# Performance work log

Hardware: AMD Instinct MI355X
Metric: run time of the kernel (lower is better)

## Reference

```python
import jax, jax.numpy as jnp
import numpy as np

EMBED_DIM = 1024
NUM_HEADS = 16
HEAD_DIM = EMBED_DIM // NUM_HEADS


def setup_inputs() -> dict:
    key = jax.random.key(0)
    ks = jax.random.split(key, 11)
    B, S, D = 4, 2048, EMBED_DIM
    s = 1.0 / np.sqrt(D)
    return {
        "q": jax.random.normal(ks[0], (B, S, D), jnp.float32),
        "k": jax.random.normal(ks[1], (B, S, D), jnp.float32),
        "v": jax.random.normal(ks[2], (B, S, D), jnp.float32),
        "Wq": jax.random.normal(ks[3], (D, D), jnp.float32) * s,
        "bq": jnp.zeros((D,), jnp.float32),
        "Wk": jax.random.normal(ks[4], (D, D), jnp.float32) * s,
        "bk": jnp.zeros((D,), jnp.float32),
        "Wv": jax.random.normal(ks[5], (D, D), jnp.float32) * s,
        "bv": jnp.zeros((D,), jnp.float32),
        "Wo": jax.random.normal(ks[6], (D, D), jnp.float32) * s,
        "bo": jnp.zeros((D,), jnp.float32),
    }


def reference(q, k, v, Wq, bq, Wk, bk, Wv, bv, Wo, bo):
    B, S, D = q.shape
    H, Hd = NUM_HEADS, HEAD_DIM
    # projections, split heads -> [B, H, S, Hd]
    qh = (q @ Wq + bq).reshape(B, S, H, Hd).transpose(0, 2, 1, 3)
    kh = (k @ Wk + bk).reshape(B, S, H, Hd).transpose(0, 2, 1, 3)
    vh = (v @ Wv + bv).reshape(B, S, H, Hd).transpose(0, 2, 1, 3)
    scale = 1.0 / jnp.sqrt(jnp.asarray(Hd, qh.dtype))
    scores = jnp.einsum('bhqd,bhkd->bhqk', qh, kh) * scale  # [B,H,S,S]
    attn = jax.nn.softmax(scores, axis=-1)  # dropout = identity in eval
    out = jnp.einsum('bhqk,bhkd->bhqd', attn, vh)
    out = out.transpose(0, 2, 1, 3).reshape(B, S, D)
    return out @ Wo + bo
```

## Files before the change

kernel.cpp:

```cpp
#include <hip/hip_runtime.h>

typedef __attribute__((ext_vector_type(8))) __bf16 bf16x8;
typedef __attribute__((ext_vector_type(4))) __bf16 bf16x4;
typedef __attribute__((ext_vector_type(4))) float f32x4;
typedef __attribute__((ext_vector_type(16))) float f32x16;
typedef __attribute__((ext_vector_type(4))) unsigned int u32x4;

#define GLDS(g, l) __builtin_amdgcn_global_load_lds( \
    (const __attribute__((address_space(1))) void*)(g), \
    (__attribute__((address_space(3))) void*)(l), 16, 0, 0)

__device__ __forceinline__ unsigned cvtpk_bf16(float lo, float hi) {
    unsigned r;
    asm("v_cvt_pk_bf16_f32 %0, %1, %2" : "=v"(r) : "v"(lo), "v"(hi));
    return r;
}
__device__ __forceinline__ void pl32swap(unsigned& a, unsigned& b) {
    asm("v_permlane32_swap_b32 %0, %1" : "+v"(a), "+v"(b));
}

__global__ __launch_bounds__(256) void cvt_tile(const float* __restrict__ q,
                                                const float* __restrict__ k,
                                                const float* __restrict__ v,
                                                __bf16* __restrict__ qo,
                                                __bf16* __restrict__ ko,
                                                __bf16* __restrict__ vo) {
    const float* src = blockIdx.z == 0 ? q : blockIdx.z == 1 ? k : v;
    __bf16* dst = blockIdx.z == 0 ? qo : blockIdx.z == 1 ? ko : vo;
    __shared__ __align__(16) __bf16 sb[128 * 64];
    const int t = threadIdx.x;
    const int m0 = blockIdx.x * 128, kk0 = blockIdx.y * 64;
    #pragma unroll
    for (int i = 0; i < 4; i++) {
        int cid = i * 256 + t;
        int r = cid >> 3, cc = cid & 7;
        const float* p = src + (size_t)(m0 + r) * 1024 + kk0 + cc * 8;
        float4 a = *(const float4*)p;
        float4 b2 = *(const float4*)(p + 4);
        bf16x8 o;
        o[0] = (__bf16)a.x;  o[1] = (__bf16)a.y;  o[2] = (__bf16)a.z;  o[3] = (__bf16)a.w;
        o[4] = (__bf16)b2.x; o[5] = (__bf16)b2.y; o[6] = (__bf16)b2.z; o[7] = (__bf16)b2.w;
        *(bf16x8*)((char*)sb + r * 128 + ((cc ^ (r & 7)) << 4)) = o;
    }
    __syncthreads();
    #pragma unroll
    for (int i = 0; i < 4; i++) {
        int cid = i * 256 + t;
        int ch = cid >> 7, r = cid & 127;
        bf16x8 o = *(const bf16x8*)((const char*)sb + r * 128 + ((ch ^ (r & 7)) << 4));
        size_t off = (((size_t)blockIdx.x * 32 + blockIdx.y * 2 + (ch >> 2)) * 4 + (ch & 3)) * 1024
                   + (size_t)r * 8;
        *(bf16x8*)(dst + off) = o;
    }
}

__global__ __launch_bounds__(256) void wtrans2(const float* __restrict__ W0,
                                               const float* __restrict__ W1,
                                               const float* __restrict__ W2,
                                               const float* __restrict__ W3,
                                               __bf16* __restrict__ O0,
                                               __bf16* __restrict__ O1,
                                               __bf16* __restrict__ O2,
                                               __bf16* __restrict__ O3) {
    const int z = blockIdx.z;
    const float* W = z == 0 ? W0 : z == 1 ? W1 : z == 2 ? W2 : W3;
    __bf16* Wt2 = z == 0 ? O0 : z == 1 ? O1 : z == 2 ? O2 : O3;
    __shared__ float lw[64][65];
    const int kt = blockIdx.y * 64, nt = blockIdx.x * 64;
    const int t = threadIdx.x;
    const int r = t >> 4;
    const int c4 = (t & 15) * 4;
    #pragma unroll
    for (int rr = 0; rr < 64; rr += 16) {
        float4 vv = *(const float4*)&W[(size_t)(kt + r + rr) * 1024 + nt + c4];
        lw[r + rr][c4 + 0] = vv.x; lw[r + rr][c4 + 1] = vv.y;
        lw[r + rr][c4 + 2] = vv.z; lw[r + rr][c4 + 3] = vv.w;
    }
    __syncthreads();
    #pragma unroll
    for (int rr = 0; rr < 64; rr += 16) {
        int n = nt + r + rr;
        bf16x4 ov;
        #pragma unroll
        for (int i = 0; i < 4; i++) ov[i] = (__bf16)lw[c4 + i][r + rr];
        int kg = kt + c4;
        size_t off = (((size_t)(n >> 7) * 32 + (kg >> 5)) * 4 + ((kg & 31) >> 3)) * 1024
                   + (size_t)(n & 127) * 8 + (kg & 7);
        *(bf16x4*)&Wt2[off] = ov;
    }
}

__global__ __launch_bounds__(256, 2)
void gemm_tt(const __bf16* __restrict__ A0, const __bf16* __restrict__ A1,
             const __bf16* __restrict__ A2,
             const __bf16* __restrict__ B0, const __bf16* __restrict__ B1,
             const __bf16* __restrict__ B2,
             const float* __restrict__ bi0, const float* __restrict__ bi1,
             const float* __restrict__ bi2,
             void* __restrict__ C0, void* __restrict__ C1, void* __restrict__ C2,
             int mode0) {
    __shared__ __align__(16) __bf16 sA[3 * 4096];
    __shared__ __align__(16) __bf16 sB[3 * 4096];
    const int y = blockIdx.y;
    const __bf16* At  = y == 0 ? A0 : y == 1 ? A1 : A2;
    const __bf16* Bt2 = y == 0 ? B0 : y == 1 ? B1 : B2;
    const float* bias = y == 0 ? bi0 : y == 1 ? bi1 : bi2;
    void* Cout        = y == 0 ? C0 : y == 1 ? C1 : C2;
    const int mode    = y == 0 ? mode0 : y + 1;

    const int t = threadIdx.x, l = t & 63, w = t >> 6;
    const int wr = w >> 1, wc = w & 1;
    const int bid = blockIdx.x, slot = bid >> 3;
    const int ytile = (bid & 7) * 8 + (slot & 7);
    const int xtile = slot >> 3;
    const __bf16* Ab = At + (size_t)ytile * 131072;
    const __bf16* Bb = Bt2 + (size_t)xtile * 131072;

#define GISSUE(ks_, buf_) do { \
    GLDS(Ab + (ks_) * 4096 + t * 8,        (char*)sA + (buf_) * 8192 + t * 16); \
    GLDS(Ab + (ks_) * 4096 + 2048 + t * 8, (char*)sA + (buf_) * 8192 + 4096 + t * 16); \
    GLDS(Bb + (ks_) * 4096 + t * 8,        (char*)sB + (buf_) * 8192 + t * 16); \
    GLDS(Bb + (ks_) * 4096 + 2048 + t * 8, (char*)sB + (buf_) * 8192 + 4096 + t * 16); \
} while (0)

    f32x4 acc[4][4];
    #pragma unroll
    for (int i = 0; i < 4; i++)
        #pragma unroll
        for (int j = 0; j < 4; j++) acc[i][j] = (f32x4){0.f, 0.f, 0.f, 0.f};

    GISSUE(0, 0);
    GISSUE(1, 1);
    int cur = 0;
    #pragma unroll 1
    for (int ks = 0; ks < 32; ++ks) {
        if (ks < 31) asm volatile("s_waitcnt vmcnt(4)" ::: "memory");
        else         asm volatile("s_waitcnt vmcnt(0)" ::: "memory");
        __builtin_amdgcn_s_barrier();
        __builtin_amdgcn_sched_barrier(0);
        if (ks + 2 < 32) GISSUE(ks + 2, cur >= 1 ? cur - 1 : 2);
        const __bf16* bA = sA + cur * 4096;
        const __bf16* bB = sB + cur * 4096;
        bf16x8 af[4], bfr[4];
        #pragma unroll
        for (int i = 0; i < 4; i++)
            af[i] = *(const bf16x8*)(bA + (l >> 4) * 1024 + (wr * 64 + i * 16 + (l & 15)) * 8);
        #pragma unroll
        for (int j = 0; j < 4; j++)
            bfr[j] = *(const bf16x8*)(bB + (l >> 4) * 1024 + (wc * 64 + j * 16 + (l & 15)) * 8);
        __builtin_amdgcn_s_setprio(1);
        #pragma unroll
        for (int i = 0; i < 4; i++)
            #pragma unroll
            for (int j = 0; j < 4; j++)
                acc[i][j] = __builtin_amdgcn_mfma_f32_16x16x32_bf16(af[i], bfr[j], acc[i][j], 0, 0, 0);
        __builtin_amdgcn_s_setprio(0);
        cur = cur == 2 ? 0 : cur + 1;
    }
#undef GISSUE

    const int m0 = ytile * 128, n0 = xtile * 128;
    #pragma unroll
    for (int j = 0; j < 4; j++) {
        int col = n0 + wc * 64 + j * 16 + (l & 15);
        float bv = bias[col];
        #pragma unroll
        for (int i = 0; i < 4; i++) {
            #pragma unroll
            for (int r = 0; r < 4; r++) {
                int row = m0 + wr * 64 + i * 16 + (l >> 4) * 4 + r;
                float vvv = acc[i][j][r] + bv;
                if (mode == 0) {
                    ((float*)Cout)[(size_t)row * 1024 + col] = vvv;
                } else if (mode == 1) {
                    ((__bf16*)Cout)[(size_t)row * 1024 + col] = (__bf16)(vvv * 0.18033688f);
                } else if (mode == 2) {
                    int b_ = row >> 11, s_ = row & 2047, h_ = col >> 6, hd_ = col & 63;
                    size_t off = ((size_t)(b_ * 16 + h_) * 32 + (s_ >> 6)) * 4096
                               + (size_t)(hd_ >> 3) * 512 + (s_ & 63) * 8 + (hd_ & 7);
                    ((__bf16*)Cout)[off] = (__bf16)vvv;
                } else {
                    int b_ = row >> 11, s_ = row & 2047, h_ = col >> 6, d_ = col & 63;
                    size_t off = ((size_t)(b_ * 16 + h_) * 32 + (s_ >> 6)) * 4096
                               + (size_t)((s_ & 63) >> 3) * 512 + (size_t)d_ * 8 + (s_ & 7);
                    ((__bf16*)Cout)[off] = (__bf16)vvv;
                }
            }
        }
    }
}

__global__ __launch_bounds__(256, 2)
void attn_fwd(const __bf16* __restrict__ Qp, const __bf16* __restrict__ Kt,
              const __bf16* __restrict__ Vtt, __bf16* __restrict__ AOt) {
    constexpr int S = 2048, D = 1024;
    __shared__ __align__(16) __bf16 sK[3 * 4096];
    __shared__ __align__(16) __bf16 sV[3 * 4096];
    const int t = threadIdx.x, l = t & 63, w = t >> 6;
    const int c = l & 31, g = l >> 5;
    const int bid = blockIdx.x, slot = bid >> 3;
    const int bh = (slot >> 3) * 8 + (bid & 7);
    const int qb = slot & 7;
    const int b = bh >> 4, h = bh & 15;
    const int q0 = qb * 256;
    const __bf16* Kb = Kt + (size_t)bh * 131072;
    const __bf16* Vb = Vtt + (size_t)bh * 131072;

    bf16x8 qf[2][4];
    #pragma unroll
    for (int qh = 0; qh < 2; qh++) {
        const __bf16* qp = Qp + (size_t)(b * S + q0 + w * 64 + qh * 32 + c) * D + h * 64;
        #pragma unroll
        for (int ks = 0; ks < 4; ks++)
            qf[qh][ks] = *(const bf16x8*)(qp + ks * 16 + g * 8);
    }
    const __bf16 one = (__bf16)1.0f;
    const bf16x8 ones = {one, one, one, one, one, one, one, one};
    asm volatile("s_waitcnt vmcnt(0)" ::: "memory");

#define AISSUE(ti_, buf_) do { \
    GLDS(Kb + (ti_) * 4096 + t * 8,        (char*)sK + (buf_) * 8192 + t * 16); \
    GLDS(Kb + (ti_) * 4096 + 2048 + t * 8, (char*)sK + (buf_) * 8192 + 4096 + t * 16); \
    GLDS(Vb + (ti_) * 4096 + t * 8,        (char*)sV + (buf_) * 8192 + t * 16); \
    GLDS(Vb + (ti_) * 4096 + 2048 + t * 8, (char*)sV + (buf_) * 8192 + 4096 + t * 16); \
} while (0)

    f32x16 acc[2][2];
    acc[0][0] = (f32x16){}; acc[0][1] = (f32x16){};
    acc[1][0] = (f32x16){}; acc[1][1] = (f32x16){};
    f32x16 accl[2];
    accl[0] = (f32x16){}; accl[1] = (f32x16){};

    AISSUE(0, 0);
    AISSUE(1, 1);
    int cur = 0;
    #pragma unroll 1
    for (int tile = 0; tile < 32; ++tile) {
        if (tile < 31) asm volatile("s_waitcnt vmcnt(4)" ::: "memory");
        else           asm volatile("s_waitcnt vmcnt(0)" ::: "memory");
        __builtin_amdgcn_s_barrier();
        __builtin_amdgcn_sched_barrier(0);
        if (tile + 2 < 32) AISSUE(tile + 2, cur >= 1 ? cur - 1 : 2);
        const __bf16* bK = sK + cur * 4096;
        const __bf16* bV = sV + cur * 4096;
        #pragma unroll
        for (int kt = 0; kt < 2; kt++) {
            bf16x8 kf[4];
            #pragma unroll
            for (int ks = 0; ks < 4; ks++)
                kf[ks] = *(const bf16x8*)(bK + ((2 * ks + g) * 64 + kt * 32 + c) * 8);
            bf16x8 vq0[2], vq1[2];
            #pragma unroll
            for (int ti = 0; ti < 2; ti++) {
                vq0[ti] = *(const bf16x8*)(bV + ((4 * kt + g) * 64 + ti * 32 + c) * 8);
                vq1[ti] = *(const bf16x8*)(bV + ((4 * kt + 2 + g) * 64 + ti * 32 + c) * 8);
            }
            #pragma unroll
            for (int qh = 0; qh < 2; qh++) {
                f32x16 St = {};
                __builtin_amdgcn_s_setprio(1);
                St = __builtin_amdgcn_mfma_f32_32x32x16_bf16(kf[0], qf[qh][0], St, 0, 0, 0);
                St = __builtin_amdgcn_mfma_f32_32x32x16_bf16(kf[1], qf[qh][1], St, 0, 0, 0);
                St = __builtin_amdgcn_mfma_f32_32x32x16_bf16(kf[2], qf[qh][2], St, 0, 0, 0);
                St = __builtin_amdgcn_mfma_f32_32x32x16_bf16(kf[3], qf[qh][3], St, 0, 0, 0);
                __builtin_amdgcn_s_setprio(0);
                #pragma unroll
                for (int r2 = 0; r2 < 16; r2++)
                    St[r2] = __builtin_amdgcn_exp2f(St[r2]);
                unsigned w0 = cvtpk_bf16(St[0], St[1]),   w1 = cvtpk_bf16(St[2], St[3]);
                unsigned w2 = cvtpk_bf16(St[4], St[5]),   w3 = cvtpk_bf16(St[6], St[7]);
                unsigned w4 = cvtpk_bf16(St[8], St[9]),   w5 = cvtpk_bf16(St[10], St[11]);
                unsigned w6 = cvtpk_bf16(St[12], St[13]), w7 = cvtpk_bf16(St[14], St[15]);
                pl32swap(w0, w2); pl32swap(w1, w3);
                pl32swap(w4, w6); pl32swap(w5, w7);
                bf16x8 pa0 = __builtin_bit_cast(bf16x8, (u32x4){w0, w1, w2, w3});
                bf16x8 pa1 = __builtin_bit_cast(bf16x8, (u32x4){w4, w5, w6, w7});
                __builtin_amdgcn_s_setprio(1);
                acc[qh][0] = __builtin_amdgcn_mfma_f32_32x32x16_bf16(pa0, vq0[0], acc[qh][0], 0, 0, 0);
                acc[qh][1] = __builtin_amdgcn_mfma_f32_32x32x16_bf16(pa0, vq0[1], acc[qh][1], 0, 0, 0);
                acc[qh][0] = __builtin_amdgcn_mfma_f32_32x32x16_bf16(pa1, vq1[0], acc[qh][0], 0, 0, 0);
                acc[qh][1] = __builtin_amdgcn_mfma_f32_32x32x16_bf16(pa1, vq1[1], acc[qh][1], 0, 0, 0);
                accl[qh] = __builtin_amdgcn_mfma_f32_32x32x16_bf16(pa0, ones, accl[qh], 0, 0, 0);
                accl[qh] = __builtin_amdgcn_mfma_f32_32x32x16_bf16(pa1, ones, accl[qh], 0, 0, 0);
                __builtin_amdgcn_s_setprio(0);
            }
        }
        cur = cur == 2 ? 0 : cur + 1;
    }
#undef AISSUE

    #pragma unroll
    for (int qh = 0; qh < 2; qh++)
        #pragma unroll
        for (int rq = 0; rq < 4; rq++)
            #pragma unroll
            for (int rr2 = 0; rr2 < 4; rr2++) {
                int reg = rq * 4 + rr2;
                int rloc = rr2 + 8 * rq + 4 * g;
                float rn = __builtin_amdgcn_rcpf(accl[qh][reg]);
                int qloc = w * 64 + qh * 32 + rloc;
                int mt = b * 16 + qb * 2 + (qloc >> 7);
                int mr = qloc & 127;
                size_t base = ((size_t)mt * 32 + h * 2) * 4096 + (size_t)(c >> 3) * 1024
                            + (size_t)mr * 8 + (c & 7);
                AOt[base] = (__bf16)(acc[qh][0][reg] * rn);
                AOt[base + 4096] = (__bf16)(acc[qh][1][reg] * rn);
            }
}

extern "C" void kernel_launch(void* const* d_in, const int* in_sizes, int n_in,
                              void* d_out, int out_size, void* d_ws, size_t ws_size,
                              hipStream_t stream) {
    const float* q  = (const float*)d_in[0];
    const float* k  = (const float*)d_in[1];
    const float* v  = (const float*)d_in[2];
    const float* Wq = (const float*)d_in[3];
    const float* bq = (const float*)d_in[4];
    const float* Wk = (const float*)d_in[5];
    const float* bk = (const float*)d_in[6];
    const float* Wv = (const float*)d_in[7];
    const float* bv = (const float*)d_in[8];
    const float* Wo = (const float*)d_in[9];
    const float* bo = (const float*)d_in[10];

    char* ws = (char*)d_ws;
    const size_t MiB = 1024 * 1024;
    __bf16* Atq = (__bf16*)(ws);
    __bf16* Atk = (__bf16*)(ws + 16 * MiB);
    __bf16* Atv = (__bf16*)(ws + 32 * MiB);
    __bf16* W2q = (__bf16*)(ws + 48 * MiB);
    __bf16* W2k = (__bf16*)(ws + 50 * MiB);
    __bf16* W2v = (__bf16*)(ws + 52 * MiB);
    __bf16* W2o = (__bf16*)(ws + 54 * MiB);
    __bf16* Qp  = (__bf16*)(ws + 56 * MiB);
    __bf16* Kt  = (__bf16*)(ws + 72 * MiB);
    __bf16* Vtt = (__bf16*)(ws + 88 * MiB);
    __bf16* AOt = (__bf16*)(ws);

    cvt_tile<<<dim3(64, 16, 3), 256, 0, stream>>>(q, k, v, Atq, Atk, Atv);

    wtrans2<<<dim3(16, 16, 4), 256, 0, stream>>>(Wq, Wk, Wv, Wo, W2q, W2k, W2v, W2o);

    gemm_tt<<<dim3(512, 3), 256, 0, stream>>>(Atq, Atk, Atv, W2q, W2k, W2v,
                                              bq, bk, bv, Qp, Kt, Vtt, 1);

    attn_fwd<<<512, 256, 0, stream>>>(Qp, Kt, Vtt, AOt);

    gemm_tt<<<dim3(512, 1), 256, 0, stream>>>(AOt, AOt, AOt, W2o, W2o, W2o,
                                              bo, bo, bo, d_out, d_out, d_out, 0);
}
```

Baseline: 205.9 us.

## Switch GEMMs to 256x128 tiles with 32x32 MFMA and move softmax rowsum to VALU

Replaces the 128x128 GEMM with a templated 512-thread kernel that computes 256x128 tiles over 64-wide K steps with 32x32x16 MFMAs. Loads are split into two phases that interleave with compute, and input and weight layouts are reformatted to match. In attention, the ones-vector MFMAs used for the row sums become VALU accumulation plus a shuffle and an LDS reciprocal table. Prefetch issue also moves to the end of each tile and setprio hints are dropped. The aim is better operand reuse and fewer MFMA instructions, at the cost of more LDS per block, larger blocks and more VALU work in attention.

Measured after the change: 202.0 us. About the same (-1.9%).

```diff
diff --git a/kernel.cpp b/kernel.cpp
--- a/kernel.cpp
+++ b/kernel.cpp
@@ -43,13 +43,14 @@
         *(bf16x8*)((char*)sb + r * 128 + ((cc ^ (r & 7)) << 4)) = o;
     }
     __syncthreads();
+    const int mt = blockIdx.x >> 1, rowbase = (blockIdx.x & 1) * 128;
     #pragma unroll
     for (int i = 0; i < 4; i++) {
         int cid = i * 256 + t;
         int ch = cid >> 7, r = cid & 127;
         bf16x8 o = *(const bf16x8*)((const char*)sb + r * 128 + ((ch ^ (r & 7)) << 4));
-        size_t off = (((size_t)blockIdx.x * 32 + blockIdx.y * 2 + (ch >> 2)) * 4 + (ch & 3)) * 1024
-                   + (size_t)r * 8;
+        size_t off = (size_t)mt * 262144 + (size_t)blockIdx.y * 16384
+                   + (size_t)ch * 2048 + (size_t)(rowbase + r) * 8;
         *(bf16x8*)(dst + off) = o;
     }
 }
@@ -84,92 +85,118 @@
         #pragma unroll
         for (int i = 0; i < 4; i++) ov[i] = (__bf16)lw[c4 + i][r + rr];
         int kg = kt + c4;
-        size_t off = (((size_t)(n >> 7) * 32 + (kg >> 5)) * 4 + ((kg & 31) >> 3)) * 1024
-                   + (size_t)(n & 127) * 8 + (kg & 7);
+        size_t off = (size_t)(n >> 7) * 131072 + (size_t)(kg >> 6) * 8192
+                   + (size_t)((kg >> 3) & 7) * 1024 + (size_t)(n & 127) * 8 + (kg & 7);
         *(bf16x4*)&Wt2[off] = ov;
     }
 }
 
-__global__ __launch_bounds__(256, 2)
-void gemm_tt(const __bf16* __restrict__ A0, const __bf16* __restrict__ A1,
+template <int QKV>
+__global__ __launch_bounds__(512, 2)
+void gemm_ph(const __bf16* __restrict__ A0, const __bf16* __restrict__ A1,
              const __bf16* __restrict__ A2,
              const __bf16* __restrict__ B0, const __bf16* __restrict__ B1,
              const __bf16* __restrict__ B2,
              const float* __restrict__ bi0, const float* __restrict__ bi1,
              const float* __restrict__ bi2,
-             void* __restrict__ C0, void* __restrict__ C1, void* __restrict__ C2,
-             int mode0) {
-    __shared__ __align__(16) __bf16 sA[3 * 4096];
-    __shared__ __align__(16) __bf16 sB[3 * 4096];
+             void* __restrict__ C0, void* __restrict__ C1, void* __restrict__ C2) {
+    __shared__ __align__(16) __bf16 sA[3 * 16384];
+    __shared__ __align__(16) __bf16 sB[3 * 8192];
+    const int t = threadIdx.x, l = t & 63;
+    const int wv = t >> 6;
+    const int wm = wv >> 1, wn = wv & 1;
     const int y = blockIdx.y;
-    const __bf16* At  = y == 0 ? A0 : y == 1 ? A1 : A2;
-    const __bf16* Bt2 = y == 0 ? B0 : y == 1 ? B1 : B2;
-    const float* bias = y == 0 ? bi0 : y == 1 ? bi1 : bi2;
-    void* Cout        = y == 0 ? C0 : y == 1 ? C1 : C2;
-    const int mode    = y == 0 ? mode0 : y + 1;
-
-    const int t = threadIdx.x, l = t & 63, w = t >> 6;
-    const int wr = w >> 1, wc = w & 1;
-    const int bid = blockIdx.x, slot = bid >> 3;
-    const int ytile = (bid & 7) * 8 + (slot & 7);
-    const int xtile = slot >> 3;
-    const __bf16* Ab = At + (size_t)ytile * 131072;
-    const __bf16* Bb = Bt2 + (size_t)xtile * 131072;
-
-#define GISSUE(ks_, buf_) do { \
-    GLDS(Ab + (ks_) * 4096 + t * 8,        (char*)sA + (buf_) * 8192 + t * 16); \
-    GLDS(Ab + (ks_) * 4096 + 2048 + t * 8, (char*)sA + (buf_) * 8192 + 4096 + t * 16); \
-    GLDS(Bb + (ks_) * 4096 + t * 8,        (char*)sB + (buf_) * 8192 + t * 16); \
-    GLDS(Bb + (ks_) * 4096 + 2048 + t * 8, (char*)sB + (buf_) * 8192 + 4096 + t * 16); \
+    const __bf16* At = QKV ? (y == 0 ? A0 : y == 1 ? A1 : A2) : A0;
+    const __bf16* Bt = QKV ? (y == 0 ? B0 : y == 1 ? B1 : B2) : B0;
+    const float* bias = QKV ? (y == 0 ? bi0 : y == 1 ? bi1 : bi2) : bi0;
+    void* Cout        = QKV ? (y == 0 ? C0 : y == 1 ? C1 : C2) : C0;
+    const int mode = QKV ? y + 1 : 0;
+
+    const int bid = blockIdx.x;
+    const int wgid = (bid & 7) * 32 + (bid >> 3);
+    const int mt = wgid >> 3, ntg = wgid & 7;
+    const __bf16* Ag = At + (size_t)mt * 262144;
+    const __bf16* Bg = Bt + (size_t)ntg * 131072;
+
+    const int aRow = ((wm * 64 + (l & 31)) << 4) + ((l >> 5) << 12);
+    const int bRow = ((wn * 64 + (l & 31)) << 4) + ((l >> 5) << 11);
+
+#define STG0(T_, nb_) do { \
+    GLDS(Ag + (T_) * 16384 + t * 8,         (char*)sA + (nb_) * 32768 + t * 16); \
+    GLDS(Ag + (T_) * 16384 + 4096 + t * 8,  (char*)sA + (nb_) * 32768 + 8192 + t * 16); \
+    GLDS(Bg + (T_) * 8192 + t * 8,          (char*)sB + (nb_) * 16384 + t * 16); \
 } while (0)
-
-    f32x4 acc[4][4];
-    #pragma unroll
-    for (int i = 0; i < 4; i++)
-        #pragma unroll
-        for (int j = 0; j < 4; j++) acc[i][j] = (f32x4){0.f, 0.f, 0.f, 0.f};
-
-    GISSUE(0, 0);
-    GISSUE(1, 1);
+#define STG1(T_, nb_) do { \
+    GLDS(Ag + (T_) * 16384 + 8192 + t * 8,  (char*)sA + (nb_) * 32768 + 16384 + t * 16); \
+    GLDS(Ag + (T_) * 16384 + 12288 + t * 8, (char*)sA + (nb_) * 32768 + 24576 + t * 16); \
+    GLDS(Bg + (T_) * 8192 + 4096 + t * 8,   (char*)sB + (nb_) * 16384 + 8192 + t * 16); \
+} while (0)
+
+    f32x16 acc[2][2];
+    acc[0][0] = (f32x16){}; acc[0][1] = (f32x16){};
+    acc[1][0] = (f32x16){}; acc[1][1] = (f32x16){};
+
+    STG0(0, 0); STG1(0, 0);
+    STG0(1, 1); STG1(1, 1);
+    asm volatile("s_waitcnt vmcnt(6)" ::: "memory");
+    __builtin_amdgcn_s_barrier();
+
     int cur = 0;
     #pragma unroll 1
-    for (int ks = 0; ks < 32; ++ks) {
-        if (ks < 31) asm volatile("s_waitcnt vmcnt(4)" ::: "memory");
-        else         asm volatile("s_waitcnt vmcnt(0)" ::: "memory");
-        __builtin_amdgcn_s_barrier();
-        __builtin_amdgcn_sched_barrier(0);
-        if (ks + 2 < 32) GISSUE(ks + 2, cur >= 1 ? cur - 1 : 2);
-        const __bf16* bA = sA + cur * 4096;
-        const __bf16* bB = sB + cur * 4096;
-        bf16x8 af[4], bfr[4];
-        #pragma unroll
-        for (int i = 0; i < 4; i++)
-            af[i] = *(const bf16x8*)(bA + (l >> 4) * 1024 + (wr * 64 + i * 16 + (l & 15)) * 8);
-        #pragma unroll
-        for (int j = 0; j < 4; j++)
-            bfr[j] = *(const bf16x8*)(bB + (l >> 4) * 1024 + (wc * 64 + j * 16 + (l & 15)) * 8);
-        __builtin_amdgcn_s_setprio(1);
-        #pragma unroll
-        for (int i = 0; i < 4; i++)
-            #pragma unroll
-            for (int j = 0; j < 4; j++)
-                acc[i][j] = __builtin_amdgcn_mfma_f32_16x16x32_bf16(af[i], bfr[j], acc[i][j], 0, 0, 0);
-        __builtin_amdgcn_s_setprio(0);
+    for (int T = 0; T < 16; ++T) {
+        const char* bA = (const char*)sA + cur * 32768;
+        const char* bB = (const char*)sB + cur * 16384;
+        const int nb = cur >= 1 ? cur - 1 : 2;
+        #pragma unroll
+        for (int ph = 0; ph < 2; ph++) {
+            bf16x8 af[2][2], bfr[2][2];
+            #pragma unroll
+            for (int ks = 0; ks < 2; ks++) {
+                int kst = ph * 2 + ks;
+                #pragma unroll
+                for (int r = 0; r < 2; r++) {
+                    af[ks][r]  = *(const bf16x8*)(bA + kst * 8192 + aRow + r * 512);
+                    bfr[ks][r] = *(const bf16x8*)(bB + kst * 4096 + bRow + r * 512);
+                }
+            }
+            if (T + 2 < 16) {
+                if (ph == 0) STG0(T + 2, nb); else STG1(T + 2, nb);
+            }
+            __builtin_amdgcn_s_barrier();
+            asm volatile("s_waitcnt lgkmcnt(0)" ::: "memory");
+            __builtin_amdgcn_sched_barrier(0);
+            __builtin_amdgcn_s_setprio(1);
+            #pragma unroll
+            for (int ks = 0; ks < 2; ks++)
+                #pragma unroll
+                for (int r = 0; r < 2; r++)
+                    #pragma unroll
+                    for (int cc = 0; cc < 2; cc++)
+                        acc[r][cc] = __builtin_amdgcn_mfma_f32_32x32x16_bf16(
+                            af[ks][r], bfr[ks][cc], acc[r][cc], 0, 0, 0);
+            __builtin_amdgcn_s_setprio(0);
+            if (ph == 1) {
+                if (T < 14) asm volatile("s_waitcnt vmcnt(6)" ::: "memory");
+                else        asm volatile("s_waitcnt vmcnt(0)" ::: "memory");
+            }
+            __builtin_amdgcn_s_barrier();
+        }
         cur = cur == 2 ? 0 : cur + 1;
     }
-#undef GISSUE
-
-    const int m0 = ytile * 128, n0 = xtile * 128;
-    #pragma unroll
-    for (int j = 0; j < 4; j++) {
-        int col = n0 + wc * 64 + j * 16 + (l & 15);
+#undef STG0
+#undef STG1
+
+    const int m0 = mt * 256, col0 = ntg * 128;
+    #pragma unroll
+    for (int cc = 0; cc < 2; cc++) {
+        int col = col0 + wn * 64 + cc * 32 + (l & 31);
         float bv = bias[col];
         #pragma unroll
-        for (int i = 0; i < 4; i++) {
-            #pragma unroll
-            for (int r = 0; r < 4; r++) {
-                int row = m0 + wr * 64 + i * 16 + (l >> 4) * 4 + r;
-                float vvv = acc[i][j][r] + bv;
+        for (int r = 0; r < 2; r++) {
+            #pragma unroll
+            for (int reg = 0; reg < 16; reg++) {
+                int row = m0 + wm * 64 + r * 32 + (reg & 3) + 8 * (reg >> 2) + 4 * (l >> 5);
+                float vvv = acc[r][cc][reg] + bv;
                 if (mode == 0) {
                     ((float*)Cout)[(size_t)row * 1024 + col] = vvv;
                 } else if (mode == 1) {
@@ -196,6 +223,7 @@
     constexpr int S = 2048, D = 1024;
     __shared__ __align__(16) __bf16 sK[3 * 4096];
     __shared__ __align__(16) __bf16 sV[3 * 4096];
+    __shared__ float sL[4][64];
     const int t = threadIdx.x, l = t & 63, w = t >> 6;
     const int c = l & 31, g = l >> 5;
     const int bid = blockIdx.x, slot = bid >> 3;
@@ -214,8 +242,6 @@
         for (int ks = 0; ks < 4; ks++)
             qf[qh][ks] = *(const bf16x8*)(qp + ks * 16 + g * 8);
     }
-    const __bf16 one = (__bf16)1.0f;
-    const bf16x8 ones = {one, one, one, one, one, one, one, one};
     asm volatile("s_waitcnt vmcnt(0)" ::: "memory");
 
 #define AISSUE(ti_, buf_) do { \
@@ -228,8 +254,7 @@
     f32x16 acc[2][2];
     acc[0][0] = (f32x16){}; acc[0][1] = (f32x16){};
     acc[1][0] = (f32x16){}; acc[1][1] = (f32x16){};
-    f32x16 accl[2];
-    accl[0] = (f32x16){}; accl[1] = (f32x16){};
+    float ls[2] = {0.f, 0.f};
 
     AISSUE(0, 0);
     AISSUE(1, 1);
@@ -240,7 +265,6 @@
         else           asm volatile("s_waitcnt vmcnt(0)" ::: "memory");
         __builtin_amdgcn_s_barrier();
         __builtin_amdgcn_sched_barrier(0);
-        if (tile + 2 < 32) AISSUE(tile + 2, cur >= 1 ? cur - 1 : 2);
         const __bf16* bK = sK + cur * 4096;
         const __bf16* bV = sV + cur * 4096;
         #pragma unroll
@@ -258,15 +282,16 @@
             #pragma unroll
             for (int qh = 0; qh < 2; qh++) {
                 f32x16 St = {};
-                __builtin_amdgcn_s_setprio(1);
                 St = __builtin_amdgcn_mfma_f32_32x32x16_bf16(kf[0], qf[qh][0], St, 0, 0, 0);
                 St = __builtin_amdgcn_mfma_f32_32x32x16_bf16(kf[1], qf[qh][1], St, 0, 0, 0);
                 St = __builtin_amdgcn_mfma_f32_32x32x16_bf16(kf[2], qf[qh][2], St, 0, 0, 0);
                 St = __builtin_amdgcn_mfma_f32_32x32x16_bf16(kf[3], qf[qh][3], St, 0, 0, 0);
-                __builtin_amdgcn_s_setprio(0);
                 #pragma unroll
-                for (int r2 = 0; r2 < 16; r2++)
-                    St[r2] = __builtin_amdgcn_exp2f(St[r2]);
+                for (int r2 = 0; r2 < 16; r2++) {
+                    float p = __builtin_amdgcn_exp2f(St[r2]);
+                    ls[qh] += p;
+                    St[r2] = p;
+                }
                 unsigned w0 = cvtpk_bf16(St[0], St[1]),   w1 = cvtpk_bf16(St[2], St[3]);
                 unsigned w2 = cvtpk_bf16(St[4], St[5]),   w3 = cvtpk_bf16(St[6], St[7]);
                 unsigned w4 = cvtpk_bf16(St[8], St[9]),   w5 = cvtpk_bf16(St[10], St[11]);
@@ -275,20 +300,23 @@
                 pl32swap(w4, w6); pl32swap(w5, w7);
                 bf16x8 pa0 = __builtin_bit_cast(bf16x8, (u32x4){w0, w1, w2, w3});
                 bf16x8 pa1 = __builtin_bit_cast(bf16x8, (u32x4){w4, w5, w6, w7});
-                __builtin_amdgcn_s_setprio(1);
                 acc[qh][0] = __builtin_amdgcn_mfma_f32_32x32x16_bf16(pa0, vq0[0], acc[qh][0], 0, 0, 0);
                 acc[qh][1] = __builtin_amdgcn_mfma_f32_32x32x16_bf16(pa0, vq0[1], acc[qh][1], 0, 0, 0);
                 acc[qh][0] = __builtin_amdgcn_mfma_f32_32x32x16_bf16(pa1, vq1[0], acc[qh][0], 0, 0, 0);
                 acc[qh][1] = __builtin_amdgcn_mfma_f32_32x32x16_bf16(pa1, vq1[1], acc[qh][1], 0, 0, 0);
-                accl[qh] = __builtin_amdgcn_mfma_f32_32x32x16_bf16(pa0, ones, accl[qh], 0, 0, 0);
-                accl[qh] = __builtin_amdgcn_mfma_f32_32x32x16_bf16(pa1, ones, accl[qh], 0, 0, 0);
-                __builtin_amdgcn_s_setprio(0);
             }
         }
+        if (tile + 2 < 32) AISSUE(tile + 2, cur >= 1 ? cur - 1 : 2);
         cur = cur == 2 ? 0 : cur + 1;
     }
 #undef AISSUE
 
+    float tt0 = ls[0] + __shfl_xor(ls[0], 32);
+    float tt1 = ls[1] + __shfl_xor(ls[1], 32);
+    if (l < 32) { sL[w][l] = 1.0f / tt0; sL[w][32 + l] = 1.0f / tt1; }
+    __syncthreads();
+
+    const int mt = b * 8 + qb;
     #pragma unroll
     for (int qh = 0; qh < 2; qh++)
         #pragma unroll
@@ -297,14 +325,12 @@
             for (int rr2 = 0; rr2 < 4; rr2++) {
                 int reg = rq * 4 + rr2;
                 int rloc = rr2 + 8 * rq + 4 * g;
-                float rn = __builtin_amdgcn_rcpf(accl[qh][reg]);
+                float rn = sL[w][qh * 32 + rloc];
                 int qloc = w * 64 + qh * 32 + rloc;
-                int mt = b * 16 + qb * 2 + (qloc >> 7);
-                int mr = qloc & 127;
-                size_t base = ((size_t)mt * 32 + h * 2) * 4096 + (size_t)(c >> 3) * 1024
-                            + (size_t)mr * 8 + (c & 7);
+                size_t base = (size_t)mt * 262144 + (size_t)h * 16384
+                            + (size_t)(c >> 3) * 2048 + (size_t)qloc * 8 + (c & 7);
                 AOt[base] = (__bf16)(acc[qh][0][reg] * rn);
-                AOt[base + 4096] = (__bf16)(acc[qh][1][reg] * rn);
+                AOt[base + 8192] = (__bf16)(acc[qh][1][reg] * rn);
             }
 }
 
@@ -341,11 +367,11 @@
 
     wtrans2<<<dim3(16, 16, 4), 256, 0, stream>>>(Wq, Wk, Wv, Wo, W2q, W2k, W2v, W2o);
 
-    gemm_tt<<<dim3(512, 3), 256, 0, stream>>>(Atq, Atk, Atv, W2q, W2k, W2v,
-                                              bq, bk, bv, Qp, Kt, Vtt, 1);
+    gemm_ph<1><<<dim3(256, 3), 512, 0, stream>>>(Atq, Atk, Atv, W2q, W2k, W2v,
+                                                 bq, bk, bv, Qp, Kt, Vtt);
 
     attn_fwd<<<512, 256, 0, stream>>>(Qp, Kt, Vtt, AOt);
 
-    gemm_tt<<<dim3(512, 1), 256, 0, stream>>>(AOt, AOt, AOt, W2o, W2o, W2o,
-                                              bo, bo, bo, d_out, d_out, d_out, 0);
-}
+    gemm_ph<0><<<dim3(256, 1), 512, 0, stream>>>(AOt, AOt, AOt, W2o, W2o, W2o,
+                                                 bo, bo, bo, d_out, d_out, d_out);
+}
```
